# Performance work log

Measured on AMD Instinct MI355X. Metric: run time of the kernel, lower is better.

Reference implementation:

```python
import jax, jax.numpy as jnp
import numpy as np

B, N, QN, C, H = 4, 1024, 512, 1024, 16
D = C // H  # head_dim = 64


def setup_inputs() -> dict:
    key = jax.random.key(0)
    ks = jax.random.split(key, 8)
    w = lambda k, shape: jax.random.normal(k, shape, jnp.float32) * 0.02
    return dict(
        x=jax.random.normal(ks[0], (B, N, C), jnp.float32),
        query=jax.random.normal(ks[1], (B, QN, C), jnp.float32),
        w_qkv=w(ks[2], (3 * C, C)),        # self.qkv (no bias)
        w_kv=w(ks[3], (2 * C, C)),         # self.to_query_kv (no bias)
        w_qlin=w(ks[4], (3 * C, C)),       # self.query_linear (no bias)
        gate=jnp.zeros((1, H, 1, 1), jnp.float32),  # zero-initialized gate param
        w_proj=w(ks[5], (C, C)),
        b_proj=jnp.zeros((C,), jnp.float32),
        w_qproj=w(ks[6], (C, C)),
        b_qproj=jnp.zeros((C,), jnp.float32),
    )


def _sdpa(q, k, v, scale):
    # q,k,v: [B,H,S,D]; standard softmax attention (attn_mask=None, p=0)
    s = jnp.einsum('bhqd,bhkd->bhqk', q, k) * scale
    return jnp.einsum('bhqk,bhkd->bhqd', jax.nn.softmax(s, axis=-1), v)


def reference(x, query, w_qkv, w_kv, w_qlin, gate, w_proj, b_proj, w_qproj, b_qproj):
    scale = 1.0 / np.sqrt(D)
    # qkv on x -> [3,B,H,N,D]
    qkv = (x @ w_qkv.T).reshape(B, N, 3, H, D).transpose(2, 0, 3, 1, 4)
    q, k, v = qkv[0], qkv[1], qkv[2]
    # kv for cross path computed from ORIGINAL x (before self-attn), as in torch code
    kv = (x @ w_kv.T).reshape(B, N, 2, H, D).transpose(2, 0, 3, 1, 4)
    xk0, xv0 = kv[0], kv[1]
    # self-attention on x (x_mask=None)
    x_attn = _sdpa(q, k, v, scale)  # [B,H,N,D]
    # query qkv -> [3,B,H,QN,D]
    qq3 = (query @ w_qlin.T).reshape(B, QN, 3, H, D).transpose(2, 0, 3, 1, 4)
    qq, qk, qv = qq3[0], qq3[1], qq3[2]
    xk = jnp.concatenate([xk0, qk], axis=2)  # [B,H,N+QN,D]
    xv = jnp.concatenate([xv0, qv], axis=2)
    scores = jnp.einsum('bhqd,bhkd->bhqk', qq, xk) * scale  # [B,H,QN,N+QN]
    # split softmax with tanh-gated first segment (mask=None; dropout p=0)
    gated = jnp.concatenate(
        [jnp.tanh(gate) * jax.nn.softmax(scores[..., :N], axis=-1),
         jax.nn.softmax(scores[..., N:], axis=-1)], axis=-1)
    q_attn = jnp.einsum('bhqk,bhkd->bhqd', gated, xv)  # [B,H,QN,D]
    x_out = x_attn.transpose(0, 2, 1, 3).reshape(B, N, C) @ w_proj.T + b_proj
    q_out = q_attn.transpose(0, 2, 1, 3).reshape(B, QN, C) @ w_qproj.T + b_qproj
    return (x_out, q_out)
```

## Files before the change

### kernel.cpp

```cpp
#include <hip/hip_runtime.h>


using bf16 = __bf16;
typedef __bf16 bf16x4 __attribute__((ext_vector_type(4)));
typedef __bf16 bf16x8 __attribute__((ext_vector_type(8)));
typedef float  f32x4  __attribute__((ext_vector_type(4)));
typedef float  f32x16 __attribute__((ext_vector_type(16)));
typedef unsigned int u32x4 __attribute__((ext_vector_type(4)));

#define MFMA16(a, b, c) __builtin_amdgcn_mfma_f32_16x16x32_bf16((a), (b), (c), 0, 0, 0)
#define MFMA32(a, b, c) __builtin_amdgcn_mfma_f32_32x32x16_bf16((a), (b), (c), 0, 0, 0)

__device__ __forceinline__ int swz128(int row) { return ((row ^ (row >> 3)) & 7) << 4; }

__device__ __forceinline__ void gl_lds16(const void* g, void* l) {
  __builtin_amdgcn_global_load_lds(
      (const __attribute__((address_space(1))) unsigned int*)g,
      (__attribute__((address_space(3))) unsigned int*)l, 16, 0, 0);
}

__device__ __forceinline__ unsigned pack2(float a, float b) {
  unsigned short ua = __builtin_bit_cast(unsigned short, (bf16)a);
  unsigned short ub = __builtin_bit_cast(unsigned short, (bf16)b);
  return (unsigned)ua | ((unsigned)ub << 16);
}

__device__ __forceinline__ float exp2_fast(float x) {
  float r;
  asm("v_exp_f32 %0, %1" : "=v"(r) : "v"(x));
  return r;
}

#define WAITV(N) asm volatile("s_waitcnt vmcnt(" #N ")" ::: "memory")
#define LGKM0()  asm volatile("s_waitcnt lgkmcnt(0)" ::: "memory")
#define SCHED0() __builtin_amdgcn_sched_barrier(0)
#define RAW_BAR() do { __builtin_amdgcn_s_barrier(); asm volatile("" ::: "memory"); } while (0)

__global__ void k_cast_all(const float* __restrict__ s0, const float* __restrict__ s1,
                           const float* __restrict__ s2, const float* __restrict__ s3,
                           const float* __restrict__ s4, const float* __restrict__ s5,
                           const float* __restrict__ s6, bf16* __restrict__ dst) {
  constexpr size_t MM = 1u << 20;
  constexpr size_t o1 = 4 * MM, o2 = 6 * MM, o3 = 9 * MM, o4 = 11 * MM,
                   o5 = 14 * MM, o6 = 15 * MM, total = 16 * MM;
  size_t stride = (size_t)gridDim.x * blockDim.x * 8;
  for (size_t i = ((size_t)blockIdx.x * blockDim.x + threadIdx.x) * 8; i < total; i += stride) {
    const float* s; size_t loc;
    if (i < o1)      { s = s0; loc = i; }
    else if (i < o2) { s = s1; loc = i - o1; }
    else if (i < o3) { s = s2; loc = i - o2; }
    else if (i < o4) { s = s3; loc = i - o3; }
    else if (i < o5) { s = s4; loc = i - o4; }
    else if (i < o6) { s = s5; loc = i - o5; }
    else             { s = s6; loc = i - o6; }
    float4 a = *(const float4*)(s + loc);
    float4 b = *(const float4*)(s + loc + 4);
    bf16x8 o;
    o[0] = (bf16)a.x; o[1] = (bf16)a.y; o[2] = (bf16)a.z; o[3] = (bf16)a.w;
    o[4] = (bf16)b.x; o[5] = (bf16)b.y; o[6] = (bf16)b.z; o[7] = (bf16)b.w;
    *(bf16x8*)(dst + i) = o;
  }
}

__global__ __launch_bounds__(512)
void k_gemm_big(const bf16* __restrict__ xb, const bf16* __restrict__ qb,
                const bf16* __restrict__ wqkvb, const bf16* __restrict__ wqlinb,
                bf16* __restrict__ XK, bf16* __restrict__ VTs, bf16* __restrict__ VT0,
                bf16* __restrict__ QQK, bf16* __restrict__ VTq) {
  constexpr int K = 1024, NT = 16;
  __shared__ bf16 As[2 * 2 * 256 * 32];
  __shared__ bf16 Bs[2 * 2 * 256 * 32];
  const int tid = threadIdx.x;
  const int lane = tid & 63, w = tid >> 6;
  const int wm = w >> 2, wn = w & 3;
  const int r0 = lane & 15, kg = lane >> 4;
  const int bid = ((int)blockIdx.x & 7) * 52 + ((int)blockIdx.x >> 3);
  int grp, tm, tn;
  const bf16 *Ap, *Bp;
  if (bid < 320) { grp = 0; tm = (bid / 20) * 256; tn = (bid % 20) * 256; Ap = xb; Bp = wqkvb; }
  else { grp = 1; int t = bid - 320; tm = (t / 12) * 256; tn = (t % 12) * 256; Ap = qb; Bp = wqlinb; }

  auto stage = [&](int T, int mat, int kh) {
    const bf16* src = mat ? Bp : Ap;
    const int t0 = mat ? tn : tm;
    char* base = (char*)(mat ? (void*)Bs : (void*)As) + (((T & 1) * 2 + kh) << 14);
#pragma unroll
    for (int i = 0; i < 2; i++) {
      int c = i * 512 + tid;
      int row = c >> 2, g = c & 3;
      int sg = (g ^ ((row >> 1) & 3)) * 8;
      gl_lds16(src + (size_t)(t0 + row) * K + T * 64 + kh * 32 + sg, base + c * 16);
    }
  };
  auto ldA = [&](int bi, int kh, int row) -> bf16x8 {
    return *(const bf16x8*)((const char*)As + ((bi * 2 + kh) << 14) + row * 64 +
                            ((kg ^ ((row >> 1) & 3)) << 4));
  };
  auto ldB = [&](int bi, int kh, int row) -> bf16x8 {
    return *(const bf16x8*)((const char*)Bs + ((bi * 2 + kh) << 14) + row * 64 +
                            ((kg ^ ((row >> 1) & 3)) << 4));
  };

  f32x4 acc[8][4] = {};

  stage(0, 0, 0); stage(0, 1, 0); stage(0, 0, 1); stage(0, 1, 1);
  stage(1, 0, 0); stage(1, 1, 0);
  WAITV(4);
  RAW_BAR();

  for (int j = 0; j < NT; ++j) {
    const int bi = j & 1;
    bf16x8 af[4], bfk[4];
#pragma unroll
    for (int i = 0; i < 4; i++) af[i] = ldA(bi, 0, wm * 128 + i * 16 + r0);
#pragma unroll
    for (int nf = 0; nf < 4; nf++) bfk[nf] = ldB(bi, 0, wn * 64 + nf * 16 + r0);
    if (j + 1 < NT) stage(j + 1, 0, 1);
    RAW_BAR(); LGKM0(); SCHED0();
    __builtin_amdgcn_s_setprio(1);
#pragma unroll
    for (int i = 0; i < 4; i++)
#pragma unroll
      for (int nf = 0; nf < 4; nf++) acc[i][nf] = MFMA16(af[i], bfk[nf], acc[i][nf]);
    __builtin_amdgcn_s_setprio(0);
    RAW_BAR();
#pragma unroll
    for (int i = 0; i < 4; i++) af[i] = ldA(bi, 0, wm * 128 + 64 + i * 16 + r0);
    if (j + 1 < NT) stage(j + 1, 1, 1);
    RAW_BAR(); LGKM0(); SCHED0();
    __builtin_amdgcn_s_setprio(1);
#pragma unroll
    for (int i = 0; i < 4; i++)
#pragma unroll
      for (int nf = 0; nf < 4; nf++) acc[4 + i][nf] = MFMA16(af[i], bfk[nf], acc[4 + i][nf]);
    __builtin_amdgcn_s_setprio(0);
    RAW_BAR();
#pragma unroll
    for (int i = 0; i < 4; i++) af[i] = ldA(bi, 1, wm * 128 + i * 16 + r0);
#pragma unroll
    for (int nf = 0; nf < 4; nf++) bfk[nf] = ldB(bi, 1, wn * 64 + nf * 16 + r0);
    if (j + 2 < NT) stage(j + 2, 0, 0);
    RAW_BAR(); LGKM0(); SCHED0();
    __builtin_amdgcn_s_setprio(1);
#pragma unroll
    for (int i = 0; i < 4; i++)
#pragma unroll
      for (int nf = 0; nf < 4; nf++) acc[i][nf] = MFMA16(af[i], bfk[nf], acc[i][nf]);
    __builtin_amdgcn_s_setprio(0);
    RAW_BAR();
#pragma unroll
    for (int i = 0; i < 4; i++) af[i] = ldA(bi, 1, wm * 128 + 64 + i * 16 + r0);
    if (j + 2 < NT) stage(j + 2, 1, 0);
    RAW_BAR(); LGKM0(); SCHED0();
    __builtin_amdgcn_s_setprio(1);
#pragma unroll
    for (int i = 0; i < 4; i++)
#pragma unroll
      for (int nf = 0; nf < 4; nf++) acc[4 + i][nf] = MFMA16(af[i], bfk[nf], acc[4 + i][nf]);
    __builtin_amdgcn_s_setprio(0);
    if (j < NT - 2) { WAITV(4); } else { WAITV(0); }
    RAW_BAR();
  }

#pragma unroll
  for (int mf = 0; mf < 8; mf++) {
    const int rowb = tm + wm * 128 + mf * 16 + kg * 4;
#pragma unroll
    for (int nf = 0; nf < 4; nf++) {
      const int coln = tn + wn * 64 + nf * 16 + r0;
      bool rm; int rmcol = coln, vbase = 0, tokb = 10, rs_ = 3072;
      bf16* vt = VTs;
      bf16* rmp = XK;
      if (grp == 0) {
        if (tn < 2048)      { rm = true; }
        else if (tn < 3072) { rm = false; vbase = 2048; vt = VTs; }
        else if (tn < 4096) { rm = true; rmcol = coln - 1024; }
        else                { rm = false; vbase = 4096; vt = VT0; }
      } else {
        rs_ = 2048; tokb = 9; rmp = QQK;
        if (tn < 2048) { rm = true; }
        else           { rm = false; vbase = 2048; vt = VTq; }
      }
      if (rm) {
#pragma unroll
        for (int j = 0; j < 4; j++)
          rmp[(size_t)(rowb + j) * rs_ + rmcol] = (bf16)acc[mf][nf][j];
      } else {
        int dg = coln - vbase, h_ = dg >> 6, dd = dg & 63;
        int bq = rowb >> tokb, tok = rowb & ((1 << tokb) - 1);
        bf16x4 wv;
#pragma unroll
        for (int j = 0; j < 4; j++) wv[j] = (bf16)acc[mf][nf][j];
        *(bf16x4*)(vt + (((size_t)((bq * 16 + h_) * 64 + dd)) << tokb) + tok) = wv;
      }
    }
  }
}

__global__ __launch_bounds__(256)
void k_gemm_proj(const bf16* __restrict__ A, const bf16* __restrict__ B0,
                 const bf16* __restrict__ B1, const float* __restrict__ bias0,
                 const float* __restrict__ bias1, float* __restrict__ OUT) {
  constexpr int K = 1024, N = 1024;
  __shared__ bf16 As[128 * 64];
  __shared__ bf16 Bs[128 * 64];
  const int tid = threadIdx.x;
  const int lane = tid & 63, w = tid >> 6;
  const int wr = w >> 1, wc = w & 1;
  const int nbx = N / 128;
  const int bid = ((int)blockIdx.x & 7) * ((int)gridDim.x >> 3) + ((int)blockIdx.x >> 3);
  const int tm = (bid / nbx) * 128, tn = (bid % nbx) * 128;
  const int r0 = lane & 15, kg = lane >> 4;
  const bf16* Bp = (tm < 4096) ? B0 : B1;
  const float* bias = (tm < 4096) ? bias0 : bias1;
  f32x4 acc[4][4] = {};
  for (int kk = 0; kk < K; kk += 64) {
#pragma unroll
    for (int i = 0; i < 4; i++) {
      int c = i * 256 + tid;
      int row = c >> 3, kb = c & 7;
      int sb = (kb ^ ((row ^ (row >> 3)) & 7)) * 8;
      gl_lds16(A + (size_t)(tm + row) * K + kk + sb, (char*)As + c * 16);
      gl_lds16(Bp + (size_t)(tn + row) * K + kk + sb, (char*)Bs + c * 16);
    }
    __syncthreads();
#pragma unroll
    for (int ks = 0; ks < 2; ks++) {
      bf16x8 af[4], bfv[4];
#pragma unroll
      for (int f = 0; f < 4; f++) {
        int rowa = wr * 64 + f * 16 + r0;
        af[f] = *(const bf16x8*)((const char*)As +
                                 ((rowa * 128 + ks * 64 + kg * 16) ^ swz128(rowa)));
        int rowb = wc * 64 + f * 16 + r0;
        bfv[f] = *(const bf16x8*)((const char*)Bs +
                                  ((rowb * 128 + ks * 64 + kg * 16) ^ swz128(rowb)));
      }
#pragma unroll
      for (int mf = 0; mf < 4; mf++)
#pragma unroll
        for (int nf = 0; nf < 4; nf++)
          acc[mf][nf] = MFMA16(af[mf], bfv[nf], acc[mf][nf]);
    }
    __syncthreads();
  }
#pragma unroll
  for (int mf = 0; mf < 4; mf++)
#pragma unroll
    for (int j = 0; j < 4; j++) {
      int row = tm + wr * 64 + mf * 16 + kg * 4 + j;
#pragma unroll
      for (int nf = 0; nf < 4; nf++) {
        int col = tn + wc * 64 + nf * 16 + r0;
        OUT[(size_t)row * 1024 + col] = acc[mf][nf][j] + bias[col];
      }
    }
}

template<int NT>
__device__ __forceinline__ void attn_pass32(
    const bf16* __restrict__ Kg, int kRS,
    const bf16* __restrict__ VTg, int vRS,
    int ntiles, const bf16x8* qf, bf16* Ks, bf16* Vt,
    f32x16* o, float& m, float& rs) {
  const int tid = threadIdx.x;
  const int lane = tid & 63;
  const int lq = lane & 31, kg2 = lane >> 5;

  auto stage = [&](int t) {
    bf16* kd = Ks + (t & 1) * 4096;
    bf16* vd = Vt + (t & 1) * 4096;
    const bf16* kt = Kg + (size_t)t * 64 * kRS;
#pragma unroll
    for (int i = 0; i < 512 / NT; i++) {
      int c = i * NT + tid;
      int r = c >> 3, kb = c & 7;
      int sb = (kb ^ ((r ^ (r >> 3)) & 7)) * 8;
      gl_lds16(kt + (size_t)r * kRS + sb, (char*)kd + c * 16);
    }
#pragma unroll
    for (int i = 0; i < 512 / NT; i++) {
      int c = i * NT + tid;
      int r = c >> 3, kb = c & 7;
      int sb = (kb ^ ((r ^ (r >> 3)) & 7)) * 8;
      gl_lds16(VTg + (size_t)r * vRS + t * 64 + sb, (char*)vd + c * 16);
    }
  };

  stage(0);
  WAITV(0);
  RAW_BAR();

  for (int t = 0; t < ntiles; t++) {
    const char* KsC = (const char*)(Ks + (t & 1) * 4096);
    const char* VtC = (const char*)(Vt + (t & 1) * 4096);
    if (t + 1 < ntiles) stage(t + 1);

    f32x16 s[2];
    s[0] = (f32x16)0.f; s[1] = (f32x16)0.f;
    __builtin_amdgcn_s_setprio(1);
#pragma unroll
    for (int kb = 0; kb < 2; kb++) {
      int row = kb * 32 + lq;
#pragma unroll
      for (int dw = 0; dw < 4; dw++) {
        bf16x8 kf = *(const bf16x8*)(KsC + ((row * 128 + dw * 32 + kg2 * 16) ^ swz128(row)));
        s[kb] = MFMA32(kf, qf[dw], s[kb]);
      }
    }
    __builtin_amdgcn_s_setprio(0);

    float mm[8];
#pragma unroll
    for (int j = 0; j < 8; j++)
      mm[j] = fmaxf(fmaxf(s[0][j], s[0][j + 8]), fmaxf(s[1][j], s[1][j + 8]));
    float a0 = fmaxf(mm[0], mm[1]), a1 = fmaxf(mm[2], mm[3]);
    float a2 = fmaxf(mm[4], mm[5]), a3 = fmaxf(mm[6], mm[7]);
    float vmax = fmaxf(fmaxf(a0, a1), fmaxf(a2, a3));
    vmax = fmaxf(vmax, __shfl_xor(vmax, 32, 64));
    if (__any(vmax > m + 11.5f)) {
      float mn = fmaxf(m, vmax);
      float fac = exp2_fast(m - mn);
      m = mn;
      rs *= fac;
#pragma unroll
      for (int j = 0; j < 16; j++) {
        int rowq = (j & 3) + 8 * (j >> 2) + 4 * kg2;
        float fj = __shfl(fac, rowq, 64);
        o[0][j] *= fj;
        o[1][j] *= fj;
      }
    }
    float t0 = 0.f, t1 = 0.f, t2 = 0.f, t3 = 0.f;
#pragma unroll
    for (int kb = 0; kb < 2; kb++)
#pragma unroll
      for (int j = 0; j < 16; j += 4) {
        float p0 = exp2_fast(s[kb][j + 0] - m);
        float p1 = exp2_fast(s[kb][j + 1] - m);
        float p2 = exp2_fast(s[kb][j + 2] - m);
        float p3 = exp2_fast(s[kb][j + 3] - m);
        s[kb][j + 0] = p0; s[kb][j + 1] = p1; s[kb][j + 2] = p2; s[kb][j + 3] = p3;
        t0 += p0; t1 += p1; t2 += p2; t3 += p3;
      }
    float tsum = (t0 + t1) + (t2 + t3);
    tsum += __shfl_xor(tsum, 32, 64);
    rs += tsum;

    unsigned pk[2][4][2];
#pragma unroll
    for (int kb = 0; kb < 2; kb++)
#pragma unroll
      for (int n = 0; n < 4; n++) {
        pk[kb][n][0] = pack2(s[kb][4 * n + 0], s[kb][4 * n + 1]);
        pk[kb][n][1] = pack2(s[kb][4 * n + 2], s[kb][4 * n + 3]);
      }

#pragma unroll
    for (int w = 0; w < 4; w++) {
      const int kb = w >> 1, wb = w & 1;
      unsigned pushA = kg2 ? pk[kb][2 * wb][0] : pk[kb][2 * wb + 1][0];
      unsigned pushB = kg2 ? pk[kb][2 * wb][1] : pk[kb][2 * wb + 1][1];
      unsigned rcvA = __shfl_xor(pushA, 32, 64);
      unsigned rcvB = __shfl_xor(pushB, 32, 64);
      u32x4 fu;
      fu[0] = kg2 ? rcvA : pk[kb][2 * wb][0];
      fu[1] = kg2 ? rcvB : pk[kb][2 * wb][1];
      fu[2] = kg2 ? pk[kb][2 * wb + 1][0] : rcvA;
      fu[3] = kg2 ? pk[kb][2 * wb + 1][1] : rcvB;
      bf16x8 pfrag = __builtin_bit_cast(bf16x8, fu);
      __builtin_amdgcn_s_setprio(1);
#pragma unroll
      for (int db = 0; db < 2; db++) {
        int d = db * 32 + lq;
        bf16x8 vf = *(const bf16x8*)(VtC + ((d * 128 + w * 32 + kg2 * 16) ^ swz128(d)));
        o[db] = MFMA32(pfrag, vf, o[db]);
      }
      __builtin_amdgcn_s_setprio(0);
    }

    WAITV(0);
    RAW_BAR();
  }
}

__global__ __launch_bounds__(256)
void k_attn(const bf16* __restrict__ XK, const bf16* __restrict__ QQK,
            const bf16* __restrict__ VTs, const bf16* __restrict__ VT0,
            const bf16* __restrict__ VTq, const float* __restrict__ gate,
            bf16* __restrict__ xat, bf16* __restrict__ qat) {
  __shared__ bf16 Ks[2 * 4096], Vt[2 * 4096];
  const int pb = blockIdx.x;
  const int bid = (pb & 7) * 96 + (pb >> 3);
  const int tid = threadIdx.x, lane = tid & 63, wv = tid >> 6;
  const int lq = lane & 31, kg2 = lane >> 5;
  constexpr float QS = 0.125f * 1.44269504088896f;

  if (bid < 512) {
    const int bh = bid >> 3, r = bid & 7;
    const int b = bh >> 4, h = bh & 15;
    const int qtok = b * 1024 + r * 128 + wv * 32;
    bf16x8 qf[4];
#pragma unroll
    for (int dw = 0; dw < 4; dw++) {
      qf[dw] = *(const bf16x8*)(XK + (size_t)(qtok + lq) * 3072 + h * 64 + dw * 16 + kg2 * 8);
#pragma unroll
      for (int e = 0; e < 8; e++) qf[dw][e] = (bf16)((float)qf[dw][e] * QS);
    }
    f32x16 o[2];
    o[0] = (f32x16)0.f; o[1] = (f32x16)0.f;
    float m = -__builtin_inff(), rs = 0.f;
    attn_pass32<256>(XK + (size_t)(b * 1024) * 3072 + 1024 + h * 64, 3072,
                     VTs + (size_t)bh * 64 * 1024, 1024,
                     16, qf, Ks, Vt, o, m, rs);
#pragma unroll
    for (int j = 0; j < 16; j++) {
      int rowq = (j & 3) + 8 * (j >> 2) + 4 * kg2;
      float rsj = __shfl(rs, rowq, 64);
      size_t base = (size_t)(qtok + rowq) * 1024 + h * 64;
      xat[base + lq] = (bf16)(o[0][j] / rsj);
      xat[base + 32 + lq] = (bf16)(o[1][j] / rsj);
    }
  } else {
    const int c = bid - 512;
    const int bh = c >> 2, qt = c & 3;
    const int b = bh >> 4, h = bh & 15;
    const int qtok = b * 512 + qt * 128 + wv * 32;
    bf16x8 qf[4];
#pragma unroll
    for (int dw = 0; dw < 4; dw++) {
      qf[dw] = *(const bf16x8*)(QQK + (size_t)(qtok + lq) * 2048 + h * 64 + dw * 16 + kg2 * 8);
#pragma unroll
      for (int e = 0; e < 8; e++) qf[dw][e] = (bf16)((float)qf[dw][e] * QS);
    }
    const float g = tanhf(gate[h]);
    unsigned pka[2][8] = {};
    f32x16 o[2];
    o[0] = (f32x16)0.f; o[1] = (f32x16)0.f;
    float m, rs;
    if (g != 0.0f) {
      m = -__builtin_inff(); rs = 0.f;
      attn_pass32<256>(XK + (size_t)(b * 1024) * 3072 + 2048 + h * 64, 3072,
                       VT0 + (size_t)bh * 64 * 1024, 1024,
                       16, qf, Ks, Vt, o, m, rs);
#pragma unroll
      for (int j2 = 0; j2 < 8; j2++) {
        int j0 = 2 * j2;
        int rq0 = (j0 & 3) + 8 * (j0 >> 2) + 4 * kg2;
        float ra = __shfl(rs, rq0, 64);
        float rb = __shfl(rs, rq0 + 1, 64);
        pka[0][j2] = pack2(g * o[0][j0] / ra, g * o[0][j0 + 1] / rb);
        pka[1][j2] = pack2(g * o[1][j0] / ra, g * o[1][j0 + 1] / rb);
      }
      o[0] = (f32x16)0.f; o[1] = (f32x16)0.f;
    }
    m = -__builtin_inff(); rs = 0.f;
    attn_pass32<256>(QQK + (size_t)(b * 512) * 2048 + 1024 + h * 64, 2048,
                     VTq + (size_t)bh * 64 * 512, 512,
                     8, qf, Ks, Vt, o, m, rs);
#pragma unroll
    for (int j = 0; j < 16; j++) {
      int rowq = (j & 3) + 8 * (j >> 2) + 4 * kg2;
      float rsj = __shfl(rs, rowq, 64);
      size_t base = (size_t)(qtok + rowq) * 1024 + h * 64;
      unsigned wa = pka[0][j >> 1], wb = pka[1][j >> 1];
      unsigned short ua = (j & 1) ? (unsigned short)(wa >> 16) : (unsigned short)(wa & 0xffffu);
      unsigned short ub = (j & 1) ? (unsigned short)(wb >> 16) : (unsigned short)(wb & 0xffffu);
      float a0 = (float)__builtin_bit_cast(bf16, ua);
      float a1 = (float)__builtin_bit_cast(bf16, ub);
      qat[base + lq] = (bf16)(o[0][j] / rsj + a0);
      qat[base + 32 + lq] = (bf16)(o[1][j] / rsj + a1);
    }
  }
}

extern "C" void kernel_launch(void* const* d_in, const int* in_sizes, int n_in,
                              void* d_out, int out_size, void* d_ws, size_t ws_size,
                              hipStream_t stream) {
  (void)in_sizes; (void)n_in; (void)out_size; (void)ws_size;
  const float* x       = (const float*)d_in[0];
  const float* query   = (const float*)d_in[1];
  const float* w_qkv   = (const float*)d_in[2];
  const float* w_kv    = (const float*)d_in[3];
  const float* w_qlin  = (const float*)d_in[4];
  const float* gate    = (const float*)d_in[5];
  const float* w_proj  = (const float*)d_in[6];
  const float* b_proj  = (const float*)d_in[7];
  const float* w_qproj = (const float*)d_in[8];
  const float* b_qproj = (const float*)d_in[9];
  float* out = (float*)d_out;

  bf16* p = (bf16*)d_ws;
  bf16* xb = p;      p += (size_t)4096 * 1024;
  bf16* qb = p;      p += (size_t)2048 * 1024;
  bf16* wqkvb = p;   p += (size_t)3072 * 1024;
  bf16* wkvb = p;    p += (size_t)2048 * 1024;
  bf16* wqlinb = p;  p += (size_t)3072 * 1024;
  bf16* wprojb = p;  p += (size_t)1024 * 1024;
  bf16* wqprojb = p; p += (size_t)1024 * 1024;
  bf16* XK = p;      p += (size_t)4096 * 3072;
  bf16* VTs = p;     p += (size_t)64 * 64 * 1024;
  bf16* VT0 = p;     p += (size_t)64 * 64 * 1024;
  bf16* QQK = p;     p += (size_t)2048 * 2048;
  bf16* VTq = p;     p += (size_t)64 * 64 * 512;
  bf16* xat = p;     p += (size_t)4096 * 1024;
  bf16* qat = p;     p += (size_t)2048 * 1024;
  (void)wkvb;

  k_cast_all<<<2048, 256, 0, stream>>>(x, query, w_qkv, w_kv, w_qlin, w_proj, w_qproj,
                                       (bf16*)d_ws);

  k_gemm_big<<<dim3(416), 512, 0, stream>>>(xb, qb, wqkvb, wqlinb,
                                            XK, VTs, VT0, QQK, VTq);

  k_attn<<<dim3(768), 256, 0, stream>>>(XK, QQK, VTs, VT0, VTq, gate, xat, qat);

  k_gemm_proj<<<dim3(48 * 8), 256, 0, stream>>>(xat, wprojb, wqprojb, b_proj, b_qproj, out);
}
```

Baseline: 178.3 us.

## Software-pipeline attention loop by overlapping PV of previous tile with QK softmax

Splits the attention tile loop into QK/softmax and PV phases. The PV matmul for tile t-1 now runs alongside the QK and softmax of tile t, with a two-tile lookahead on global-to-LDS staging. V tiles get a triple-buffered LDS ring so the buffer still being read is not overwritten. The goal is to keep MFMA units busy during the exp and reduction work, at the cost of extra LDS (V buffer grows to three tiles), more live registers for the packed probabilities, and possible occupancy loss.

```diff
diff --git a/kernel.cpp b/kernel.cpp
--- a/kernel.cpp
+++ b/kernel.cpp
@@ -257,7 +257,7 @@
     }
 }
 
-template<int NT>
+template<int NTH>
 __device__ __forceinline__ void attn_pass32(
     const bf16* __restrict__ Kg, int kRS,
     const bf16* __restrict__ VTg, int vRS,
@@ -267,35 +267,29 @@
   const int lane = tid & 63;
   const int lq = lane & 31, kg2 = lane >> 5;
 
-  auto stage = [&](int t) {
+  auto stageKV = [&](int t) {
     bf16* kd = Ks + (t & 1) * 4096;
-    bf16* vd = Vt + (t & 1) * 4096;
+    bf16* vd = Vt + (t % 3) * 4096;
     const bf16* kt = Kg + (size_t)t * 64 * kRS;
 #pragma unroll
-    for (int i = 0; i < 512 / NT; i++) {
-      int c = i * NT + tid;
+    for (int i = 0; i < 512 / NTH; i++) {
+      int c = i * NTH + tid;
       int r = c >> 3, kb = c & 7;
       int sb = (kb ^ ((r ^ (r >> 3)) & 7)) * 8;
       gl_lds16(kt + (size_t)r * kRS + sb, (char*)kd + c * 16);
     }
 #pragma unroll
-    for (int i = 0; i < 512 / NT; i++) {
-      int c = i * NT + tid;
+    for (int i = 0; i < 512 / NTH; i++) {
+      int c = i * NTH + tid;
       int r = c >> 3, kb = c & 7;
       int sb = (kb ^ ((r ^ (r >> 3)) & 7)) * 8;
       gl_lds16(VTg + (size_t)r * vRS + t * 64 + sb, (char*)vd + c * 16);
     }
   };
 
-  stage(0);
-  WAITV(0);
-  RAW_BAR();
-
-  for (int t = 0; t < ntiles; t++) {
-    const char* KsC = (const char*)(Ks + (t & 1) * 4096);
-    const char* VtC = (const char*)(Vt + (t & 1) * 4096);
-    if (t + 1 < ntiles) stage(t + 1);
-
+  unsigned pkp[2][4][2];
+
+  auto qk_softmax = [&](const char* KsC) {
     f32x16 s[2];
     s[0] = (f32x16)0.f; s[1] = (f32x16)0.f;
     __builtin_amdgcn_s_setprio(1);
@@ -309,7 +303,6 @@
       }
     }
     __builtin_amdgcn_s_setprio(0);
-
     float mm[8];
 #pragma unroll
     for (int j = 0; j < 8; j++)
@@ -346,28 +339,28 @@
     float tsum = (t0 + t1) + (t2 + t3);
     tsum += __shfl_xor(tsum, 32, 64);
     rs += tsum;
-
-    unsigned pk[2][4][2];
 #pragma unroll
     for (int kb = 0; kb < 2; kb++)
 #pragma unroll
       for (int n = 0; n < 4; n++) {
-        pk[kb][n][0] = pack2(s[kb][4 * n + 0], s[kb][4 * n + 1]);
-        pk[kb][n][1] = pack2(s[kb][4 * n + 2], s[kb][4 * n + 3]);
-      }
-
+        pkp[kb][n][0] = pack2(s[kb][4 * n + 0], s[kb][4 * n + 1]);
+        pkp[kb][n][1] = pack2(s[kb][4 * n + 2], s[kb][4 * n + 3]);
+      }
+  };
+
+  auto pv = [&](const char* VtC) {
 #pragma unroll
     for (int w = 0; w < 4; w++) {
       const int kb = w >> 1, wb = w & 1;
-      unsigned pushA = kg2 ? pk[kb][2 * wb][0] : pk[kb][2 * wb + 1][0];
-      unsigned pushB = kg2 ? pk[kb][2 * wb][1] : pk[kb][2 * wb + 1][1];
+      unsigned pushA = kg2 ? pkp[kb][2 * wb][0] : pkp[kb][2 * wb + 1][0];
+      unsigned pushB = kg2 ? pkp[kb][2 * wb][1] : pkp[kb][2 * wb + 1][1];
       unsigned rcvA = __shfl_xor(pushA, 32, 64);
       unsigned rcvB = __shfl_xor(pushB, 32, 64);
       u32x4 fu;
-      fu[0] = kg2 ? rcvA : pk[kb][2 * wb][0];
-      fu[1] = kg2 ? rcvB : pk[kb][2 * wb][1];
-      fu[2] = kg2 ? pk[kb][2 * wb + 1][0] : rcvA;
-      fu[3] = kg2 ? pk[kb][2 * wb + 1][1] : rcvB;
+      fu[0] = kg2 ? rcvA : pkp[kb][2 * wb][0];
+      fu[1] = kg2 ? rcvB : pkp[kb][2 * wb][1];
+      fu[2] = kg2 ? pkp[kb][2 * wb + 1][0] : rcvA;
+      fu[3] = kg2 ? pkp[kb][2 * wb + 1][1] : rcvB;
       bf16x8 pfrag = __builtin_bit_cast(bf16x8, fu);
       __builtin_amdgcn_s_setprio(1);
 #pragma unroll
@@ -378,10 +371,24 @@
       }
       __builtin_amdgcn_s_setprio(0);
     }
-
+  };
+
+  RAW_BAR();
+  stageKV(0);
+  if (ntiles > 1) { stageKV(1); WAITV(4); } else { WAITV(0); }
+  RAW_BAR();
+  qk_softmax((const char*)(Ks + 0));
+
+  for (int t = 1; t < ntiles; t++) {
     WAITV(0);
     RAW_BAR();
+    if (t + 1 < ntiles) stageKV(t + 1);
+    const char* KsC = (const char*)(Ks + (t & 1) * 4096);
+    const char* VtP = (const char*)(Vt + ((t - 1) % 3) * 4096);
+    pv(VtP);
+    qk_softmax(KsC);
   }
+  pv((const char*)(Vt + ((ntiles - 1) % 3) * 4096));
 }
 
 __global__ __launch_bounds__(256)
@@ -389,7 +396,7 @@
             const bf16* __restrict__ VTs, const bf16* __restrict__ VT0,
             const bf16* __restrict__ VTq, const float* __restrict__ gate,
             bf16* __restrict__ xat, bf16* __restrict__ qat) {
-  __shared__ bf16 Ks[2 * 4096], Vt[2 * 4096];
+  __shared__ bf16 Ks[2 * 4096], Vt[3 * 4096];
   const int pb = blockIdx.x;
   const int bid = (pb & 7) * 96 + (pb >> 3);
   const int tid = threadIdx.x, lane = tid & 63, wv = tid >> 6;
```

New measurement: 174.3 us, median of 2. -2.2%, faster.
